# Optimization experiments

Measured on AMD Instinct MI355X. Metric: run time of the kernel, lower is better.

The kernel has to match this reference:

```python
import jax, jax.numpy as jnp
import numpy as np

D_MODEL = 1024
HEADS = 16
D_K = D_MODEL // HEADS


def setup_inputs() -> dict:
    key = jax.random.key(0)
    ks = jax.random.split(key, 9)
    s = 1.0 / np.sqrt(D_MODEL)
    x = jax.random.normal(ks[0], (4, 2048, D_MODEL), dtype=jnp.float32)
    Wq = jax.random.uniform(ks[1], (D_MODEL, D_MODEL), jnp.float32, -s, s)
    Wk = jax.random.uniform(ks[2], (D_MODEL, D_MODEL), jnp.float32, -s, s)
    Wv = jax.random.uniform(ks[3], (D_MODEL, D_MODEL), jnp.float32, -s, s)
    Wo = jax.random.uniform(ks[4], (D_MODEL, D_MODEL), jnp.float32, -s, s)
    bq = jax.random.uniform(ks[5], (D_MODEL,), jnp.float32, -s, s)
    bk = jax.random.uniform(ks[6], (D_MODEL,), jnp.float32, -s, s)
    bv = jax.random.uniform(ks[7], (D_MODEL,), jnp.float32, -s, s)
    bo = jax.random.uniform(ks[8], (D_MODEL,), jnp.float32, -s, s)
    return {"x": x, "Wq": Wq, "bq": bq, "Wk": Wk, "bk": bk,
            "Wv": Wv, "bv": bv, "Wo": Wo, "bo": bo}


def reference(x, Wq, bq, Wk, bk, Wv, bv, Wo, bo):
    B, T, C = x.shape
    H, d_k = HEADS, D_K
    # QKV projections (weights stored as [in, out] -> x @ W + b)
    q = (x @ Wq + bq).reshape(B, T, H, d_k).transpose(0, 2, 1, 3)  # [B,H,T,d_k]
    k = (x @ Wk + bk).reshape(B, T, H, d_k).transpose(0, 2, 1, 3)
    v = (x @ Wv + bv).reshape(B, T, H, d_k).transpose(0, 2, 1, 3)
    scores = jnp.einsum('bhqd,bhkd->bhqk', q, k) / jnp.sqrt(jnp.float32(d_k))
    attn = jax.nn.softmax(scores, axis=-1)
    out = jnp.einsum('bhqk,bhkd->bhqd', attn, v)  # [B,H,T,d_k]
    out = out.transpose(0, 2, 1, 3).reshape(B, T, C)
    return out @ Wo + bo
```

## Files before the change

### kernel.cpp

```cpp
#include <hip/hip_runtime.h>
#include <stdint.h>

typedef _Float16 f16;
typedef _Float16 f16x8 __attribute__((ext_vector_type(8)));
typedef float    f32x4 __attribute__((ext_vector_type(4)));
typedef unsigned int u32x4 __attribute__((ext_vector_type(4)));
typedef unsigned int u32x2 __attribute__((ext_vector_type(2)));
typedef unsigned short u16;

#define MFMA16(A,B,C) __builtin_amdgcn_mfma_f32_16x16x32_f16(A,B,C,0,0,0)

__device__ __forceinline__ void gload_lds16(const void* g, void* l) {
  auto gp = reinterpret_cast<const __attribute__((address_space(1))) unsigned int*>(
      reinterpret_cast<uintptr_t>(g));
  auto lp = reinterpret_cast<__attribute__((address_space(3))) unsigned int*>(
      reinterpret_cast<uintptr_t>(l));
  __builtin_amdgcn_global_load_lds(gp, lp, 16, 0, 0);
}

__device__ __forceinline__ unsigned pk16(float a, float b) {
  unsigned short ua = __builtin_bit_cast(unsigned short, (f16)a);
  unsigned short ub = __builtin_bit_cast(unsigned short, (f16)b);
  return ((unsigned)ub << 16) | (unsigned)ua;
}
__device__ __forceinline__ unsigned pk2rtz(float a, float b) {
  return __builtin_bit_cast(unsigned, __builtin_amdgcn_cvt_pkrtz(a, b));
}
__device__ __forceinline__ float ex2(float x) {
  float r; asm("v_exp_f32 %0, %1" : "=v"(r) : "v"(x)); return r;
}
__device__ __forceinline__ f16x8 asf16(u32x4 v) { return __builtin_bit_cast(f16x8, v); }

#define LOG2E 1.44269504088896f

__global__ __launch_bounds__(256) void k_prep(const float* __restrict__ x, u16* __restrict__ xb,
                                              const float* __restrict__ Wq, const float* __restrict__ Wk,
                                              const float* __restrict__ Wv, const float* __restrict__ Wo,
                                              u16* __restrict__ WTq, u16* __restrict__ WTk,
                                              u16* __restrict__ WTv, u16* __restrict__ WTo) {
  __shared__ float tile[64][65];
  int tid = threadIdx.x;
  if (blockIdx.x < 4096) {
    int i = blockIdx.x * 256 + tid;
    const float4* p = (const float4*)x + (size_t)i * 2;
    float4 a = p[0], b = p[1];
    u32x4 o = { pk16(a.x, a.y), pk16(a.z, a.w), pk16(b.x, b.y), pk16(b.z, b.w) };
    *((u32x4*)xb + i) = o;
    return;
  }
  int bid = blockIdx.x - 4096;
  int z = bid >> 8;
  const float* W = (z == 0) ? Wq : (z == 1) ? Wk : (z == 2) ? Wv : Wo;
  u16* WT = (z == 0) ? WTq : (z == 1) ? WTk : (z == 2) ? WTv : WTo;
  int r0 = ((bid >> 4) & 15) * 64, c0 = (bid & 15) * 64;
#pragma unroll
  for (int i = 0; i < 4; ++i) {
    int idx = tid + i * 256;
    int row = idx >> 4, ch = (idx & 15) * 4;
    float4 v = *(const float4*)&W[(size_t)(r0 + row) * 1024 + c0 + ch];
    tile[row][ch + 0] = v.x; tile[row][ch + 1] = v.y;
    tile[row][ch + 2] = v.z; tile[row][ch + 3] = v.w;
  }
  __syncthreads();
#pragma unroll
  for (int i = 0; i < 4; ++i) {
    int idx = tid + i * 256;
    int orow = idx >> 4, ch = (idx & 15) * 4;
    u32x2 o = { pk16(tile[ch + 0][orow], tile[ch + 1][orow]),
                pk16(tile[ch + 2][orow], tile[ch + 3][orow]) };
    *(u32x2*)&WT[(size_t)(c0 + orow) * 1024 + r0 + ch] = o;
  }
}

__device__ __forceinline__ void gemm_core(const u16* __restrict__ A, const u16* __restrict__ B,
                                          u16* sA, u16* sB, int m0, int n0, f32x4 acc[4][4]) {
  const int tid = threadIdx.x;
  const int lane = tid & 63;
  const int w = tid >> 6;
  const int wr = w >> 2, wc = w & 3;
  const int c = lane & 15, g = lane >> 4;
#pragma unroll
  for (int i = 0; i < 4; ++i)
#pragma unroll
    for (int j = 0; j < 4; ++j) acc[i][j] = (f32x4){0.f, 0.f, 0.f, 0.f};

  auto stage = [&](int buf, int kt) {
    {
      int L = tid * 16;
      int row = L >> 6;
      int chl = (L >> 4) & 3;
      int chg = chl ^ ((row >> 1) & 3);
      gload_lds16(A + (size_t)(m0 + row) * 1024 + kt + chg * 8, (char*)sA + buf * 8192 + L);
    }
#pragma unroll
    for (int j = 0; j < 2; ++j) {
      int L = j * 8192 + tid * 16;
      int row = L >> 6;
      int chl = (L >> 4) & 3;
      int chg = chl ^ ((row >> 1) & 3);
      gload_lds16(B + (size_t)(n0 + row) * 1024 + kt + chg * 8, (char*)sB + buf * 16384 + L);
    }
  };

  stage(0, 0);
  stage(1, 32);
  int cur = 0;
  for (int kt = 0; kt < 1024; kt += 32) {
    if (kt < 1024 - 32) {
      asm volatile("s_waitcnt vmcnt(3)" ::: "memory");
    } else {
      asm volatile("s_waitcnt vmcnt(0)" ::: "memory");
    }
    __builtin_amdgcn_s_barrier();
    if (kt + 64 < 1024) {
      int nb = cur + 2; if (nb >= 3) nb -= 3;
      stage(nb, kt + 64);
    }
    const char* cA = (const char*)sA + cur * 8192;
    const char* cB = (const char*)sB + cur * 16384;
    u32x4 av[4], bv[4];
#pragma unroll
    for (int mi = 0; mi < 4; ++mi) {
      int row = wr * 64 + mi * 16 + c;
      av[mi] = *(const u32x4*)(cA + row * 64 + ((g ^ ((row >> 1) & 3)) << 4));
    }
#pragma unroll
    for (int ni = 0; ni < 4; ++ni) {
      int row = wc * 64 + ni * 16 + c;
      bv[ni] = *(const u32x4*)(cB + row * 64 + ((g ^ ((row >> 1) & 3)) << 4));
    }
#pragma unroll
    for (int mi = 0; mi < 4; ++mi)
#pragma unroll
      for (int ni = 0; ni < 4; ++ni)
        acc[mi][ni] = MFMA16(asf16(av[mi]), asf16(bv[ni]), acc[mi][ni]);
    cur = (cur == 2) ? 0 : cur + 1;
  }
}

__global__ __launch_bounds__(512, 4) void k_qkv(const u16* __restrict__ xb,
                                             const u16* __restrict__ wtq, const u16* __restrict__ wtk,
                                             const u16* __restrict__ wtv,
                                             const float* __restrict__ bq, const float* __restrict__ bk,
                                             const float* __restrict__ bv,
                                             u16* __restrict__ Qb, u16* __restrict__ Kb,
                                             u16* __restrict__ VTb) {
  __shared__ alignas(16) u16 sA[3 * 128 * 32];
  __shared__ alignas(16) u16 sB[3 * 256 * 32];
  int m0 = blockIdx.x * 128;
  int nt = blockIdx.y;
  int wsel = nt >> 2;
  int n0 = (nt & 3) * 256;
  const u16* WT = (wsel == 0) ? wtq : (wsel == 1) ? wtk : wtv;
  const float* bias = (wsel == 0) ? bq : (wsel == 1) ? bk : bv;
  f32x4 acc[4][4];
  gemm_core(xb, WT, sA, sB, m0, n0, acc);

  const int lane = threadIdx.x & 63;
  const int w = threadIdx.x >> 6;
  const int wr = w >> 2, wc = w & 3, c = lane & 15, g = lane >> 4;
#pragma unroll
  for (int mi = 0; mi < 4; ++mi) {
#pragma unroll
    for (int ni = 0; ni < 4; ++ni) {
      int ncol = n0 + wc * 64 + ni * 16 + c;
      float bcol = bias[ncol];
      int h = ncol >> 6, d = ncol & 63;
#pragma unroll
      for (int e = 0; e < 4; ++e) {
        int m = m0 + wr * 64 + mi * 16 + g * 4 + e;
        int b = m >> 11, t = m & 2047;
        int bh = (b << 4) | h;
        float val = acc[mi][ni][e] + bcol;
        if (wsel == 0) {
          Qb[((size_t)bh * 2048 + t) * 64 + d] = __builtin_bit_cast(u16, (f16)(val * (0.125f * LOG2E)));
        } else if (wsel == 1) {
          Kb[((size_t)bh * 2048 + t) * 64 + d] = __builtin_bit_cast(u16, (f16)val);
        } else {
          VTb[((size_t)bh * 64 + d) * 2048 + t] = __builtin_bit_cast(u16, (f16)val);
        }
      }
    }
  }
}

__global__ __launch_bounds__(256) void k_attn(const u16* __restrict__ Qb, const u16* __restrict__ Kb,
                                              const u16* __restrict__ VTb, u16* __restrict__ Ob) {
  __shared__ alignas(16) u16 Ks[2][64 * 64];
  __shared__ alignas(16) u16 VTs[2][64 * 64];
  const int tid = threadIdx.x, lane = tid & 63, w = tid >> 6;
  const int c = lane & 15, g = lane >> 4;
  const int lin = blockIdx.x;
  const int bh = (lin & 7) * 8 + (lin >> 7);
  const int qblk = (lin >> 3) & 15;
  const int qw = qblk * 128 + w * 32;
  const size_t kbase = (size_t)bh * 2048 * 64;
  const size_t vbase = (size_t)bh * 64 * 2048;

  u32x4 qa0 = *(const u32x4*)(Qb + ((size_t)bh * 2048 + qw + c) * 64 + g * 8);
  u32x4 qa1 = *(const u32x4*)(Qb + ((size_t)bh * 2048 + qw + c) * 64 + 32 + g * 8);
  u32x4 qa2 = *(const u32x4*)(Qb + ((size_t)bh * 2048 + qw + 16 + c) * 64 + g * 8);
  u32x4 qa3 = *(const u32x4*)(Qb + ((size_t)bh * 2048 + qw + 16 + c) * 64 + 32 + g * 8);

  const u32x4 ONES = { 0x3C003C00u, 0x3C003C00u, 0x3C003C00u, 0x3C003C00u };

  const int L0 = tid * 16, L1 = 4096 + tid * 16;
  const int row0 = L0 >> 7, row1 = L1 >> 7;
  const int chg0 = ((L0 >> 4) & 7) ^ (row0 & 7);
  const int chg1 = ((L1 >> 4) & 7) ^ (row1 & 7);
  const int vchg0 = (chg0 & 4) | ((chg0 & 1) << 1) | ((chg0 >> 1) & 1);
  const int vchg1 = (chg1 & 4) | ((chg1 & 1) << 1) | ((chg1 >> 1) & 1);
  const u16* kg0 = Kb + kbase + (size_t)row0 * 64 + chg0 * 8;
  const u16* kg1 = Kb + kbase + (size_t)row1 * 64 + chg1 * 8;
  const u16* vg0 = VTb + vbase + (size_t)row0 * 2048 + vchg0 * 8;
  const u16* vg1 = VTb + vbase + (size_t)row1 * 2048 + vchg1 * 8;

  auto stage = [&](int buf, int kt) {
    gload_lds16(kg0 + (size_t)kt * 64, (char*)Ks[buf] + L0);
    gload_lds16(kg1 + (size_t)kt * 64, (char*)Ks[buf] + L1);
    gload_lds16(vg0 + kt,              (char*)VTs[buf] + L0);
    gload_lds16(vg1 + kt,              (char*)VTs[buf] + L1);
  };

  const int A0 = c * 128 + ((g ^ (c & 7)) << 4);
  const int A1 = A0 ^ 0x40;

  f32x4 oa[2][4];
  f32x4 la[2];
#pragma unroll
  for (int qb = 0; qb < 2; ++qb) {
    la[qb] = (f32x4){0.f, 0.f, 0.f, 0.f};
#pragma unroll
    for (int i = 0; i < 4; ++i) oa[qb][i] = (f32x4){0.f, 0.f, 0.f, 0.f};
  }

  stage(0, 0);
  __syncthreads();
  int cur = 0;
  for (int kt = 0; kt < 2048; kt += 64) {
    if (kt + 64 < 2048) stage(cur ^ 1, kt + 64);

    unsigned wds[2][8];
    __builtin_amdgcn_s_setprio(1);
    const char* cK = (const char*)Ks[cur];
#pragma unroll
    for (int kb = 0; kb < 4; ++kb) {
      const char* bp = cK + kb * 2048;
      u32x4 k0 = *(const u32x4*)(bp + A0);
      u32x4 k1 = *(const u32x4*)(bp + A1);
      f32x4 z0 = (f32x4){0.f, 0.f, 0.f, 0.f};
      z0 = MFMA16(asf16(k0), asf16(qa0), z0);
      z0 = MFMA16(asf16(k1), asf16(qa1), z0);
      wds[0][kb * 2]     = pk2rtz(ex2(z0[0]), ex2(z0[1]));
      wds[0][kb * 2 + 1] = pk2rtz(ex2(z0[2]), ex2(z0[3]));
      f32x4 z1 = (f32x4){0.f, 0.f, 0.f, 0.f};
      z1 = MFMA16(asf16(k0), asf16(qa2), z1);
      z1 = MFMA16(asf16(k1), asf16(qa3), z1);
      wds[1][kb * 2]     = pk2rtz(ex2(z1[0]), ex2(z1[1]));
      wds[1][kb * 2 + 1] = pk2rtz(ex2(z1[2]), ex2(z1[3]));
    }
    __builtin_amdgcn_s_setprio(0);

    u32x4 pb0[2], pb1[2];
#pragma unroll
    for (int qb = 0; qb < 2; ++qb) {
      unsigned m0 = wds[qb][0], n0 = wds[qb][2];
      unsigned m1 = wds[qb][1], n1 = wds[qb][3];
      unsigned m2 = wds[qb][4], n2 = wds[qb][6];
      unsigned m3 = wds[qb][5], n3 = wds[qb][7];
      asm("v_permlane16_swap_b32 %0, %1" : "+v"(m0), "+v"(n0));
      asm("v_permlane16_swap_b32 %0, %1" : "+v"(m1), "+v"(n1));
      asm("v_permlane16_swap_b32 %0, %1" : "+v"(m2), "+v"(n2));
      asm("v_permlane16_swap_b32 %0, %1" : "+v"(m3), "+v"(n3));
      pb0[qb] = (u32x4){ m0, m1, n0, n1 };
      pb1[qb] = (u32x4){ m2, m3, n2, n3 };
    }

    __builtin_amdgcn_s_setprio(1);
    const char* cV = (const char*)VTs[cur];
#pragma unroll
    for (int db = 0; db < 4; ++db) {
      const char* vp = cV + db * 2048;
      u32x4 v0 = *(const u32x4*)(vp + A0);
      u32x4 v1 = *(const u32x4*)(vp + A1);
      oa[0][db] = MFMA16(asf16(v0), asf16(pb0[0]), oa[0][db]);
      oa[0][db] = MFMA16(asf16(v1), asf16(pb1[0]), oa[0][db]);
      oa[1][db] = MFMA16(asf16(v0), asf16(pb0[1]), oa[1][db]);
      oa[1][db] = MFMA16(asf16(v1), asf16(pb1[1]), oa[1][db]);
    }
    la[0] = MFMA16(asf16(ONES), asf16(pb0[0]), la[0]);
    la[0] = MFMA16(asf16(ONES), asf16(pb1[0]), la[0]);
    la[1] = MFMA16(asf16(ONES), asf16(pb0[1]), la[1]);
    la[1] = MFMA16(asf16(ONES), asf16(pb1[1]), la[1]);
    __builtin_amdgcn_s_setprio(0);

    __syncthreads();
    cur ^= 1;
  }

  int b = bh >> 4, h = bh & 15;
#pragma unroll
  for (int qb = 0; qb < 2; ++qb) {
    float inv = 1.0f / la[qb][0];
    size_t obase = ((size_t)(b * 2048 + qw + qb * 16 + c)) * 1024 + h * 64;
#pragma unroll
    for (int db = 0; db < 4; ++db) {
      int d = db * 16 + g * 4;
      u32x2 o = { pk16(oa[qb][db][0] * inv, oa[qb][db][1] * inv),
                  pk16(oa[qb][db][2] * inv, oa[qb][db][3] * inv) };
      *(u32x2*)(Ob + obase + d) = o;
    }
  }
}

__global__ __launch_bounds__(512, 4) void k_oproj(const u16* __restrict__ Ob, const u16* __restrict__ wto,
                                               const float* __restrict__ bo, float* __restrict__ out) {
  __shared__ alignas(16) u16 sA[3 * 128 * 32];
  __shared__ alignas(16) u16 sB[3 * 256 * 32];
  int m0 = blockIdx.x * 128;
  int n0 = blockIdx.y * 256;
  f32x4 acc[4][4];
  gemm_core(Ob, wto, sA, sB, m0, n0, acc);

  const int lane = threadIdx.x & 63;
  const int w = threadIdx.x >> 6;
  const int wr = w >> 2, wc = w & 3, c = lane & 15, g = lane >> 4;
#pragma unroll
  for (int mi = 0; mi < 4; ++mi) {
#pragma unroll
    for (int ni = 0; ni < 4; ++ni) {
      int ncol = n0 + wc * 64 + ni * 16 + c;
      float bcol = bo[ncol];
#pragma unroll
      for (int e = 0; e < 4; ++e) {
        int m = m0 + wr * 64 + mi * 16 + g * 4 + e;
        out[(size_t)m * 1024 + ncol] = acc[mi][ni][e] + bcol;
      }
    }
  }
}

extern "C" void kernel_launch(void* const* d_in, const int* in_sizes, int n_in,
                              void* d_out, int out_size, void* d_ws, size_t ws_size,
                              hipStream_t stream) {
  const float* x  = (const float*)d_in[0];
  const float* Wq = (const float*)d_in[1];
  const float* bq = (const float*)d_in[2];
  const float* Wk = (const float*)d_in[3];
  const float* bk = (const float*)d_in[4];
  const float* Wv = (const float*)d_in[5];
  const float* bv = (const float*)d_in[6];
  const float* Wo = (const float*)d_in[7];
  const float* bo = (const float*)d_in[8];
  float* out = (float*)d_out;
  char* ws = (char*)d_ws;

  u16* xb  = (u16*)(ws + 0);
  u16* Ob  = (u16*)(ws + 0);
  u16* wtq = (u16*)(ws + 16777216);
  u16* wtk = (u16*)(ws + 18874368);
  u16* wtv = (u16*)(ws + 20971520);
  u16* wto = (u16*)(ws + 23068672);
  u16* Qb  = (u16*)(ws + 25165824);
  u16* Kb  = (u16*)(ws + 41943040);
  u16* VTb = (u16*)(ws + 58720256);

  k_prep<<<5120, 256, 0, stream>>>(x, xb, Wq, Wk, Wv, Wo, wtq, wtk, wtv, wto);
  k_qkv<<<dim3(64, 12), 512, 0, stream>>>(xb, wtq, wtk, wtv, bq, bk, bv, Qb, Kb, VTb);
  k_attn<<<1024, 256, 0, stream>>>(Qb, Kb, VTb, Ob);
  k_oproj<<<dim3(64, 4), 512, 0, stream>>>(Ob, wto, bo, out);
}
```

Baseline: 189.1 us.

## Split GEMM k-step into two phases with interleaved prefetch and MFMA priority

Splits each k-iteration of the shared GEMM core into two halves. The A tile and first half of B are prefetched before the first half of MFMAs, and the second B prefetch is issued after a mid-iteration barrier before the second half. s_setprio is raised around MFMA blocks. The aim is to spread global-to-LDS loads among compute and favour MFMA issue. It adds an extra barrier per iteration, and the vmcnt(3) wait still assumes three loads per stage.

```diff
diff --git a/kernel.cpp b/kernel.cpp
--- a/kernel.cpp
+++ b/kernel.cpp
@@ -84,26 +84,29 @@
 #pragma unroll
     for (int j = 0; j < 4; ++j) acc[i][j] = (f32x4){0.f, 0.f, 0.f, 0.f};
 
-  auto stage = [&](int buf, int kt) {
+  auto stage_p0 = [&](int buf, int kt) {
     {
       int L = tid * 16;
       int row = L >> 6;
-      int chl = (L >> 4) & 3;
-      int chg = chl ^ ((row >> 1) & 3);
+      int chg = ((L >> 4) & 3) ^ ((row >> 1) & 3);
       gload_lds16(A + (size_t)(m0 + row) * 1024 + kt + chg * 8, (char*)sA + buf * 8192 + L);
     }
-#pragma unroll
-    for (int j = 0; j < 2; ++j) {
-      int L = j * 8192 + tid * 16;
+    {
+      int L = tid * 16;
       int row = L >> 6;
-      int chl = (L >> 4) & 3;
-      int chg = chl ^ ((row >> 1) & 3);
+      int chg = ((L >> 4) & 3) ^ ((row >> 1) & 3);
       gload_lds16(B + (size_t)(n0 + row) * 1024 + kt + chg * 8, (char*)sB + buf * 16384 + L);
     }
   };
-
-  stage(0, 0);
-  stage(1, 32);
+  auto stage_p1 = [&](int buf, int kt) {
+    int L = 8192 + tid * 16;
+    int row = L >> 6;
+    int chg = ((L >> 4) & 3) ^ ((row >> 1) & 3);
+    gload_lds16(B + (size_t)(n0 + row) * 1024 + kt + chg * 8, (char*)sB + buf * 16384 + L);
+  };
+
+  stage_p0(0, 0);  stage_p1(0, 0);
+  stage_p0(1, 32); stage_p1(1, 32);
   int cur = 0;
   for (int kt = 0; kt < 1024; kt += 32) {
     if (kt < 1024 - 32) {
@@ -112,10 +115,9 @@
       asm volatile("s_waitcnt vmcnt(0)" ::: "memory");
     }
     __builtin_amdgcn_s_barrier();
-    if (kt + 64 < 1024) {
-      int nb = cur + 2; if (nb >= 3) nb -= 3;
-      stage(nb, kt + 64);
-    }
+    int nb = cur + 2; if (nb >= 3) nb -= 3;
+    const bool pf = (kt + 64 < 1024);
+    if (pf) stage_p0(nb, kt + 64);
     const char* cA = (const char*)sA + cur * 8192;
     const char* cB = (const char*)sB + cur * 16384;
     u32x4 av[4], bv[4];
@@ -125,15 +127,31 @@
       av[mi] = *(const u32x4*)(cA + row * 64 + ((g ^ ((row >> 1) & 3)) << 4));
     }
 #pragma unroll
-    for (int ni = 0; ni < 4; ++ni) {
+    for (int ni = 0; ni < 2; ++ni) {
       int row = wc * 64 + ni * 16 + c;
       bv[ni] = *(const u32x4*)(cB + row * 64 + ((g ^ ((row >> 1) & 3)) << 4));
     }
+    __builtin_amdgcn_s_setprio(1);
 #pragma unroll
     for (int mi = 0; mi < 4; ++mi)
 #pragma unroll
-      for (int ni = 0; ni < 4; ++ni)
+      for (int ni = 0; ni < 2; ++ni)
         acc[mi][ni] = MFMA16(asf16(av[mi]), asf16(bv[ni]), acc[mi][ni]);
+    __builtin_amdgcn_s_setprio(0);
+    __builtin_amdgcn_s_barrier();
+    if (pf) stage_p1(nb, kt + 64);
+#pragma unroll
+    for (int ni = 2; ni < 4; ++ni) {
+      int row = wc * 64 + ni * 16 + c;
+      bv[ni] = *(const u32x4*)(cB + row * 64 + ((g ^ ((row >> 1) & 3)) << 4));
+    }
+    __builtin_amdgcn_s_setprio(1);
+#pragma unroll
+    for (int mi = 0; mi < 4; ++mi)
+#pragma unroll
+      for (int ni = 2; ni < 4; ++ni)
+        acc[mi][ni] = MFMA16(asf16(av[mi]), asf16(bv[ni]), acc[mi][ni]);
+    __builtin_amdgcn_s_setprio(0);
     cur = (cur == 2) ? 0 : cur + 1;
   }
 }
```

Result: no change. 189.4 us (+0.2%).
